# Performance work log

Measured on AMD Instinct MI355X. Metric: run time of the kernel, lower is better.

Reference implementation:

```python
import jax, jax.numpy as jnp
from jax import lax
import numpy as np

N, E = 64, 126            # nodes per graph, directed edges (N = E//2 + 1)
BS, T = 32, 512           # batch, train_seq_len
G = BS * T                # total graphs
IN = N * 2                # encoder input_size
H8 = 128 * 8              # hidden_size * 8
OUT = 128                 # output_size (decoder GRU hidden)
L = 2                     # num_layers


def setup_inputs() -> dict:
    key = jax.random.key(0)
    ks = iter(jax.random.split(key, 64))
    def rn(shape, s=0.05):
        return jax.random.normal(next(ks), shape, dtype=jnp.float32) * s
    inp = {}
    inp['x'] = rn((G, N, 2), 1.0)
    inp['edge_index'] = jax.random.randint(next(ks), (2, E), 0, N)
    # GCN params (GCNConv(2,4), GCNConv(4,2), classifier Linear(2,2))
    inp['gcn_w1'] = rn((2, 4), 0.5); inp['gcn_b1'] = rn((4,))
    inp['gcn_w2'] = rn((4, 2), 0.5); inp['gcn_b2'] = rn((2,))
    inp['gcn_cw'] = rn((2, 2), 0.5); inp['gcn_cb'] = rn((2,))
    # Encoder: fl Linear(IN, H8); GRU(H8, H8, L)
    inp['enc_fl_w'] = rn((IN, H8)); inp['enc_fl_b'] = rn((H8,))
    inp['enc_wih'] = rn((L, 3 * H8, H8)); inp['enc_whh'] = rn((L, 3 * H8, H8))
    inp['enc_bih'] = rn((L, 3 * H8)); inp['enc_bhh'] = rn((L, 3 * H8))
    # Decoder: fl Linear(H8, H8); GRU(H8, OUT, L); Linear(OUT, OUT)
    inp['dec_fl_w'] = rn((H8, H8)); inp['dec_fl_b'] = rn((H8,))
    inp['dec_wih0'] = rn((3 * OUT, H8)); inp['dec_wih1'] = rn((3 * OUT, OUT))
    inp['dec_whh'] = rn((L, 3 * OUT, OUT))
    inp['dec_bih'] = rn((L, 3 * OUT)); inp['dec_bhh'] = rn((L, 3 * OUT))
    inp['dec_lin_w'] = rn((OUT, OUT)); inp['dec_lin_b'] = rn((OUT,))
    return inp


def _gcn_conv(h, src, dst, W, b):
    # PyG GCNConv: self-loops + symmetric normalization. h: [G, N, Fin]
    hw = h @ W                                   # [G, N, Fout]
    deg = jnp.ones((N,), hw.dtype).at[dst].add(jnp.ones((E,), hw.dtype))
    dinv = lax.rsqrt(deg)
    norm = dinv[src] * dinv[dst]                 # [E]
    msgs = hw[:, src, :] * norm[None, :, None]   # gather + scale
    agg = jnp.zeros_like(hw).at[:, dst, :].add(msgs)
    agg = agg + hw * (dinv * dinv)[None, :, None]  # self-loop term (norm = 1/deg)
    return agg + b


def _gru_layer(x_seq, wih, whh, bih, bhh):
    # x_seq: [B, T, D]; torch nn.GRU math, h0 = 0
    B = x_seq.shape[0]
    H = whh.shape[1]
    h0 = jnp.zeros((B, H), x_seq.dtype)
    def step(h, x_t):
        gi = x_t @ wih.T + bih
        gh = h @ whh.T + bhh
        i_r, i_z, i_n = jnp.split(gi, 3, axis=-1)
        h_r, h_z, h_n = jnp.split(gh, 3, axis=-1)
        r = jax.nn.sigmoid(i_r + h_r)
        z = jax.nn.sigmoid(i_z + h_z)
        n = jnp.tanh(i_n + r * h_n)
        h_new = (1.0 - z) * n + z * h
        return h_new, h_new
    _, ys = lax.scan(step, h0, jnp.swapaxes(x_seq, 0, 1))
    return jnp.swapaxes(ys, 0, 1)


def reference(x, edge_index, gcn_w1, gcn_b1, gcn_w2, gcn_b2, gcn_cw, gcn_cb,
              enc_fl_w, enc_fl_b, enc_wih, enc_whh, enc_bih, enc_bhh,
              dec_fl_w, dec_fl_b, dec_wih0, dec_wih1, dec_whh, dec_bih, dec_bhh,
              dec_lin_w, dec_lin_b):
    src, dst = edge_index[0], edge_index[1]
    # GCN over all G graphs at once (vectorizes the per-graph Python loop)
    h = jnp.tanh(_gcn_conv(x, src, dst, gcn_w1, gcn_b1))
    h = jnp.tanh(_gcn_conv(h, src, dst, gcn_w2, gcn_b2))
    h = h @ gcn_cw + gcn_cb                      # [G, N, 2]
    res = h.reshape(BS, T, IN)
    # Encoder
    out = jax.nn.relu(res @ enc_fl_w + enc_fl_b)
    for l in range(L):
        out = _gru_layer(out, enc_wih[l], enc_whh[l], enc_bih[l], enc_bhh[l])
    # Decoder (dropout in eval mode = identity)
    d = jax.nn.relu(out @ dec_fl_w + dec_fl_b)
    d = _gru_layer(d, dec_wih0, dec_whh[0], dec_bih[0], dec_bhh[0])
    d = _gru_layer(d, dec_wih1, dec_whh[1], dec_bih[1], dec_bhh[1])
    return d @ dec_lin_w + dec_lin_b             # [BS, T, OUT]
```

## Files before the change

kernel.cpp:

```cpp
#include <hip/hip_runtime.h>

typedef unsigned short u16;
typedef unsigned long long u64;
typedef __attribute__((ext_vector_type(8))) short bf16x8;
typedef __attribute__((ext_vector_type(4))) float f32x4;

#define BSZ 32
#define TT 512
#define GG (BSZ*TT)
#define NNODE 64
#define EE 126
#define H8 1024
#define H3 3072

__device__ __forceinline__ float b2f(u16 u){
  union { unsigned i; float f; } v; v.i = ((unsigned)u) << 16; return v.f;
}
__device__ __forceinline__ u16 f2b(float f){
  unsigned i = __float_as_uint(f);
  unsigned r = (i + 0x7FFFu + ((i >> 16) & 1u)) >> 16;
  return (u16)r;
}
__device__ __forceinline__ float sigm(float x){ return 1.f/(1.f+__expf(-x)); }
__device__ __forceinline__ float tanh_f(float x){
  float xc = fminf(fmaxf(x, -15.f), 15.f);
  float e = __expf(2.f*xc);
  return (e-1.f)/(e+1.f);
}
__device__ __forceinline__ int prow(int m, int perm){
  return perm ? ((m & (TT-1))*BSZ + (m >> 9)) : m;
}
__device__ __forceinline__ u64 aload64(const u64* p){
  return __hip_atomic_load(p, __ATOMIC_RELAXED, __HIP_MEMORY_SCOPE_AGENT);
}
__device__ __forceinline__ void spin128(int* base, int t){
  for (;;){
    int s = 0;
    #pragma unroll
    for (int i = 0; i < 8; i++)
      s += __hip_atomic_load(&base[i*TT + t], __ATOMIC_RELAXED, __HIP_MEMORY_SCOPE_AGENT);
    if (s == 128) break;
    __builtin_amdgcn_s_sleep(1);
  }
  asm volatile("" ::: "memory");
}

__global__ __launch_bounds__(256) void detect_dtype(const void* xraw, int* flag){
  __shared__ int cnt;
  if (threadIdx.x == 0) cnt = 0;
  __syncthreads();
  const u16* p = (const u16*)xraw;
  u16 u = p[2*threadIdx.x];
  int e = (u >> 7) & 0xFF;
  int weird = (e < 100 || e > 134) ? 1 : 0;
  atomicAdd(&cnt, weird);
  __syncthreads();
  if (threadIdx.x == 0) *flag = (cnt > 128) ? 1 : 0;
}

__global__ __launch_bounds__(256) void cvt_bf16(const void* __restrict__ in,
                                                u16* __restrict__ out, int n,
                                                const int* __restrict__ flag){
  int i = blockIdx.x*256 + threadIdx.x;
  if (i >= n) return;
  if (*flag) out[i] = f2b(((const float*)in)[i]);
  else       out[i] = ((const u16*)in)[i];
}

__global__ __launch_bounds__(64) void gcn_kernel(
    const u16* __restrict__ x, const int* __restrict__ ei,
    const u16* __restrict__ w1, const u16* __restrict__ b1,
    const u16* __restrict__ w2, const u16* __restrict__ b2,
    const u16* __restrict__ cw, const u16* __restrict__ cb,
    u16* __restrict__ res)
{
  __shared__ int se[EE], de[EE];
  __shared__ float dinv[NNODE];
  __shared__ float nrm[EE];
  __shared__ float hs[NNODE][4];
  const int n = threadIdx.x;
  const int g = blockIdx.x;
  for (int e = n; e < EE; e += 64){ se[e] = ei[e]; de[e] = ei[EE + e]; }
  __syncthreads();
  int cnt = 0;
  for (int e = 0; e < EE; e++) cnt += (de[e] == n) ? 1 : 0;
  float di = rsqrtf(1.0f + (float)cnt);
  dinv[n] = di;
  float x0 = b2f(x[((size_t)g*NNODE + n)*2 + 0]);
  float x1 = b2f(x[((size_t)g*NNODE + n)*2 + 1]);
  float hw[4];
  #pragma unroll
  for (int c = 0; c < 4; c++) hw[c] = x0*b2f(w1[c]) + x1*b2f(w1[4+c]);
  #pragma unroll
  for (int c = 0; c < 4; c++) hs[n][c] = hw[c];
  __syncthreads();
  for (int e = n; e < EE; e += 64) nrm[e] = dinv[se[e]] * dinv[de[e]];
  __syncthreads();
  float selfc = di*di;
  float agg[4];
  #pragma unroll
  for (int c = 0; c < 4; c++) agg[c] = hw[c]*selfc;
  for (int e = 0; e < EE; e++){
    if (de[e] == n){
      float w = nrm[e]; int s = se[e];
      #pragma unroll
      for (int c = 0; c < 4; c++) agg[c] += hs[s][c]*w;
    }
  }
  float h1[4];
  #pragma unroll
  for (int c = 0; c < 4; c++) h1[c] = tanh_f(agg[c] + b2f(b1[c]));
  __syncthreads();
  float hw2[2];
  #pragma unroll
  for (int c = 0; c < 2; c++){
    float s = 0.f;
    #pragma unroll
    for (int k = 0; k < 4; k++) s += h1[k]*b2f(w2[k*2+c]);
    hw2[c] = s;
    hs[n][c] = s;
  }
  __syncthreads();
  float agg2[2] = { hw2[0]*selfc, hw2[1]*selfc };
  for (int e = 0; e < EE; e++){
    if (de[e] == n){
      float w = nrm[e]; int s = se[e];
      agg2[0] += hs[s][0]*w;
      agg2[1] += hs[s][1]*w;
    }
  }
  float h2a = tanh_f(agg2[0] + b2f(b2[0]));
  float h2b = tanh_f(agg2[1] + b2f(b2[1]));
  #pragma unroll
  for (int c = 0; c < 2; c++){
    float o = h2a*b2f(cw[c]) + h2b*b2f(cw[2+c]) + b2f(cb[c]);
    res[(size_t)g*128 + n*2 + c] = f2b(o);
  }
}

__global__ __launch_bounds__(256) void transpose_bf16(
    const u16* __restrict__ in, u16* __restrict__ out, int R, int C)
{
  __shared__ u16 tile[32][33];
  int c0 = blockIdx.x*32, r0 = blockIdx.y*32;
  for (int i = threadIdx.y; i < 32; i += 8)
    tile[i][threadIdx.x] = in[(size_t)(r0+i)*C + c0 + threadIdx.x];
  __syncthreads();
  for (int i = threadIdx.y; i < 32; i += 8)
    out[(size_t)(c0+i)*R + r0 + threadIdx.x] = tile[threadIdx.x][i];
}

__global__ __launch_bounds__(256) void gemm_nt(
    const u16* __restrict__ A, const u16* __restrict__ Bm,
    const u16* __restrict__ bias, void* __restrict__ C,
    int M, int N, int K, int relu, int permA, int permC,
    const int* __restrict__ outflag)
{
  const int wave = threadIdx.x >> 6;
  const int lane = threadIdx.x & 63;
  const int wm = wave >> 1, wn = wave & 1;
  const int q = lane >> 4, lr = lane & 15;
  const int mBase = blockIdx.y*128 + wm*64;
  const int nBase = blockIdx.x*128 + wn*64;
  f32x4 acc[4][4] = {};
  const u16* ap[4]; const u16* bp[4];
  #pragma unroll
  for (int i = 0; i < 4; i++){
    ap[i] = A + (size_t)prow(mBase + i*16 + lr, permA)*K + q*8;
    bp[i] = Bm + (size_t)(nBase + i*16 + lr)*K + q*8;
  }
  for (int kb = 0; kb < K; kb += 32){
    bf16x8 av[4], bv[4];
    #pragma unroll
    for (int i = 0; i < 4; i++){
      av[i] = *(const bf16x8*)ap[i]; bv[i] = *(const bf16x8*)bp[i];
      ap[i] += 32; bp[i] += 32;
    }
    #pragma unroll
    for (int mi = 0; mi < 4; mi++)
      #pragma unroll
      for (int ni = 0; ni < 4; ni++)
        acc[mi][ni] = __builtin_amdgcn_mfma_f32_16x16x32_bf16(av[mi], bv[ni], acc[mi][ni], 0, 0, 0);
  }
  const int of32 = outflag ? *outflag : 0;
  #pragma unroll
  for (int ni = 0; ni < 4; ni++){
    int col = nBase + ni*16 + lr;
    float bb = bias ? b2f(bias[col]) : 0.f;
    #pragma unroll
    for (int mi = 0; mi < 4; mi++){
      #pragma unroll
      for (int r = 0; r < 4; r++){
        int row = prow(mBase + mi*16 + q*4 + r, permC);
        float v = acc[mi][ni][r] + bb;
        if (relu) v = fmaxf(v, 0.f);
        size_t idx = (size_t)row*N + col;
        if (of32) ((float*)C)[idx] = v;
        else      ((u16*)C)[idx]   = f2b(v);
      }
    }
  }
}

__global__ __launch_bounds__(64) void enc_pipe(
    const u16* __restrict__ gi,
    const u16* __restrict__ wih1,
    const u16* __restrict__ whh0,
    const u16* __restrict__ whh1,
    const u16* __restrict__ bih1, const u16* __restrict__ bhh0,
    const u16* __restrict__ bhh1,
    u16* __restrict__ h0seq,
    u16* __restrict__ h1seq,
    int* __restrict__ cnt)
{
  const int wid = blockIdx.x;
  const int lane = threadIdx.x & 63;
  const int q = lane >> 4, lr = lane & 15;
  const int sub = wid & 7;
  float hreg[4] = {0.f,0.f,0.f,0.f};
  int* c0 = cnt;
  int* c1 = cnt + 8*TT;

  if (wid < 128){
    const int jg = wid & 63, half = wid >> 6;
    const int j = jg*16 + lr, bbase = half*16;
    const float bh_r = b2f(bhh0[j]);
    const float bh_z = b2f(bhh0[H8 + j]);
    const float bh_n = b2f(bhh0[2*H8 + j]);
    const u16* wp0 = whh0 + (size_t)(0*H8 + j)*H8 + q*8;
    const u16* wp1 = whh0 + (size_t)(1*H8 + j)*H8 + q*8;
    const u16* wp2 = whh0 + (size_t)(2*H8 + j)*H8 + q*8;
    u16 gpre[12];
    #pragma unroll
    for (int r = 0; r < 4; r++){
      size_t row = (size_t)(bbase + q*4 + r)*H3;
      gpre[r]   = gi[row + j];
      gpre[4+r] = gi[row + H8 + j];
      gpre[8+r] = gi[row + 2*H8 + j];
    }
    for (int t = 0; t < TT; t++){
      if (t > 0) spin128(c0, t - 1);
      float gr_[4], gz_[4], gn_[4];
      #pragma unroll
      for (int r = 0; r < 4; r++){
        gr_[r] = b2f(gpre[r]); gz_[r] = b2f(gpre[4+r]); gn_[r] = b2f(gpre[8+r]);
      }
      f32x4 acc0 = {}, acc1 = {}, acc2 = {};
      if (t > 0){
        const u16* ap = h0seq + (size_t)((t-1)*BSZ + bbase + lr)*H8 + q*8;
        #pragma unroll 8
        for (int kb = 0; kb < 32; kb++){
          const u64* p = (const u64*)(ap + kb*32);
          union { u64 v[2]; bf16x8 b; } A; A.v[0] = aload64(p); A.v[1] = aload64(p+1);
          bf16x8 w0 = *(const bf16x8*)(wp0 + kb*32);
          bf16x8 w1 = *(const bf16x8*)(wp1 + kb*32);
          bf16x8 w2 = *(const bf16x8*)(wp2 + kb*32);
          acc0 = __builtin_amdgcn_mfma_f32_16x16x32_bf16(A.b, w0, acc0, 0,0,0);
          acc1 = __builtin_amdgcn_mfma_f32_16x16x32_bf16(A.b, w1, acc1, 0,0,0);
          acc2 = __builtin_amdgcn_mfma_f32_16x16x32_bf16(A.b, w2, acc2, 0,0,0);
        }
      }
      #pragma unroll
      for (int r = 0; r < 4; r++){
        float rr = sigm(gr_[r] + acc0[r] + bh_r);
        float zz = sigm(gz_[r] + acc1[r] + bh_z);
        float nn = tanh_f(gn_[r] + rr*(acc2[r] + bh_n));
        float hnew = (1.f - zz)*nn + zz*hreg[r];
        hreg[r] = hnew;
        __hip_atomic_store(&h0seq[(size_t)(t*BSZ + bbase + q*4 + r)*H8 + j], f2b(hnew),
                           __ATOMIC_RELAXED, __HIP_MEMORY_SCOPE_AGENT);
      }
      asm volatile("s_waitcnt vmcnt(0)" ::: "memory");
      if (lane == 0)
        __hip_atomic_fetch_add(&c0[sub*TT + t], 1, __ATOMIC_RELAXED, __HIP_MEMORY_SCOPE_AGENT);
      if (t + 1 < TT){
        #pragma unroll
        for (int r = 0; r < 4; r++){
          size_t row = (size_t)((t+1)*BSZ + bbase + q*4 + r)*H3;
          gpre[r]   = gi[row + j];
          gpre[4+r] = gi[row + H8 + j];
          gpre[8+r] = gi[row + 2*H8 + j];
        }
      }
    }
  } else {
    const int wid2 = wid - 128;
    const int jg = wid2 & 63, half = wid2 >> 6;
    const int j = jg*16 + lr, bbase = half*16;
    const float bir = b2f(bih1[j]);
    const float biz = b2f(bih1[H8 + j]);
    const float bin = b2f(bih1[2*H8 + j]);
    const float bhr = b2f(bhh1[j]);
    const float bhz = b2f(bhh1[H8 + j]);
    const float bhn = b2f(bhh1[2*H8 + j]);
    const u16* ip0 = wih1 + (size_t)(0*H8 + j)*H8 + q*8;
    const u16* ip1 = wih1 + (size_t)(1*H8 + j)*H8 + q*8;
    const u16* ip2 = wih1 + (size_t)(2*H8 + j)*H8 + q*8;
    const u16* hp0 = whh1 + (size_t)(0*H8 + j)*H8 + q*8;
    const u16* hp1 = whh1 + (size_t)(1*H8 + j)*H8 + q*8;
    const u16* hp2 = whh1 + (size_t)(2*H8 + j)*H8 + q*8;
    for (int t = 0; t < TT; t++){
      spin128(c0, t);
      if (t > 0) spin128(c1, t - 1);
      f32x4 aI0 = {}, aI1 = {}, aI2 = {}, aH0 = {}, aH1 = {}, aH2 = {};
      const u16* a0p = h0seq + (size_t)(t*BSZ + bbase + lr)*H8 + q*8;
      if (t > 0){
        const u16* a1p = h1seq + (size_t)((t-1)*BSZ + bbase + lr)*H8 + q*8;
        #pragma unroll 4
        for (int kb = 0; kb < 32; kb++){
          const u64* p0 = (const u64*)(a0p + kb*32);
          union { u64 v[2]; bf16x8 b; } A0; A0.v[0] = aload64(p0); A0.v[1] = aload64(p0+1);
          const u64* p1 = (const u64*)(a1p + kb*32);
          union { u64 v[2]; bf16x8 b; } A1; A1.v[0] = aload64(p1); A1.v[1] = aload64(p1+1);
          bf16x8 i0 = *(const bf16x8*)(ip0 + kb*32);
          bf16x8 i1 = *(const bf16x8*)(ip1 + kb*32);
          bf16x8 i2 = *(const bf16x8*)(ip2 + kb*32);
          bf16x8 h0v = *(const bf16x8*)(hp0 + kb*32);
          bf16x8 h1v = *(const bf16x8*)(hp1 + kb*32);
          bf16x8 h2v = *(const bf16x8*)(hp2 + kb*32);
          aI0 = __builtin_amdgcn_mfma_f32_16x16x32_bf16(A0.b, i0, aI0, 0,0,0);
          aI1 = __builtin_amdgcn_mfma_f32_16x16x32_bf16(A0.b, i1, aI1, 0,0,0);
          aI2 = __builtin_amdgcn_mfma_f32_16x16x32_bf16(A0.b, i2, aI2, 0,0,0);
          aH0 = __builtin_amdgcn_mfma_f32_16x16x32_bf16(A1.b, h0v, aH0, 0,0,0);
          aH1 = __builtin_amdgcn_mfma_f32_16x16x32_bf16(A1.b, h1v, aH1, 0,0,0);
          aH2 = __builtin_amdgcn_mfma_f32_16x16x32_bf16(A1.b, h2v, aH2, 0,0,0);
        }
      } else {
        #pragma unroll 8
        for (int kb = 0; kb < 32; kb++){
          const u64* p0 = (const u64*)(a0p + kb*32);
          union { u64 v[2]; bf16x8 b; } A0; A0.v[0] = aload64(p0); A0.v[1] = aload64(p0+1);
          bf16x8 i0 = *(const bf16x8*)(ip0 + kb*32);
          bf16x8 i1 = *(const bf16x8*)(ip1 + kb*32);
          bf16x8 i2 = *(const bf16x8*)(ip2 + kb*32);
          aI0 = __builtin_amdgcn_mfma_f32_16x16x32_bf16(A0.b, i0, aI0, 0,0,0);
          aI1 = __builtin_amdgcn_mfma_f32_16x16x32_bf16(A0.b, i1, aI1, 0,0,0);
          aI2 = __builtin_amdgcn_mfma_f32_16x16x32_bf16(A0.b, i2, aI2, 0,0,0);
        }
      }
      #pragma unroll
      for (int r = 0; r < 4; r++){
        float rr = sigm(aI0[r] + bir + aH0[r] + bhr);
        float zz = sigm(aI1[r] + biz + aH1[r] + bhz);
        float nn = tanh_f(aI2[r] + bin + rr*(aH2[r] + bhn));
        float hnew = (1.f - zz)*nn + zz*hreg[r];
        hreg[r] = hnew;
        __hip_atomic_store(&h1seq[(size_t)(t*BSZ + bbase + q*4 + r)*H8 + j], f2b(hnew),
                           __ATOMIC_RELAXED, __HIP_MEMORY_SCOPE_AGENT);
      }
      asm volatile("s_waitcnt vmcnt(0)" ::: "memory");
      if (lane == 0)
        __hip_atomic_fetch_add(&c1[sub*TT + t], 1, __ATOMIC_RELAXED, __HIP_MEMORY_SCOPE_AGENT);
    }
  }
}

__global__ __launch_bounds__(256) void dec_rec(
    const u16* __restrict__ gi,
    const u16* __restrict__ whh,
    const u16* __restrict__ bhh,
    u16* __restrict__ seq)
{
  __shared__ u16 hlds[16*136];
  const int bb = blockIdx.x*16;
  const int tid = threadIdx.x;
  const int w = tid >> 6, lane = tid & 63, q = lane >> 4, lr = lane & 15;
  bf16x8 wreg[3][2][4];
  #pragma unroll
  for (int g2 = 0; g2 < 3; g2++)
    #pragma unroll
    for (int nt = 0; nt < 2; nt++){
      int jj = g2*128 + w*32 + nt*16 + lr;
      #pragma unroll
      for (int kb = 0; kb < 4; kb++)
        wreg[g2][nt][kb] = *(const bf16x8*)(whh + (size_t)jj*128 + kb*32 + q*8);
    }
  float bh[3][2];
  #pragma unroll
  for (int g2 = 0; g2 < 3; g2++)
    #pragma unroll
    for (int nt = 0; nt < 2; nt++)
      bh[g2][nt] = b2f(bhh[g2*128 + w*32 + nt*16 + lr]);
  float hreg[2][4] = {};
  u16 gpre[3][2][4];
  #pragma unroll
  for (int r = 0; r < 4; r++){
    size_t row = (size_t)(bb + q*4 + r)*384;
    #pragma unroll
    for (int nt = 0; nt < 2; nt++){
      int jj = w*32 + nt*16 + lr;
      #pragma unroll
      for (int g2 = 0; g2 < 3; g2++)
        gpre[g2][nt][r] = gi[row + g2*128 + jj];
    }
  }
  __syncthreads();
  for (int t = 0; t < TT; t++){
    float gif[3][2][4];
    #pragma unroll
    for (int g2 = 0; g2 < 3; g2++)
      #pragma unroll
      for (int nt = 0; nt < 2; nt++)
        #pragma unroll
        for (int r = 0; r < 4; r++)
          gif[g2][nt][r] = b2f(gpre[g2][nt][r]);
    f32x4 acc[3][2] = {};
    if (t > 0){
      #pragma unroll
      for (int kb = 0; kb < 4; kb++){
        bf16x8 a = *(const bf16x8*)(hlds + lr*136 + kb*32 + q*8);
        #pragma unroll
        for (int g2 = 0; g2 < 3; g2++)
          #pragma unroll
          for (int nt = 0; nt < 2; nt++)
            acc[g2][nt] = __builtin_amdgcn_mfma_f32_16x16x32_bf16(a, wreg[g2][nt][kb], acc[g2][nt], 0,0,0);
      }
    }
    __syncthreads();
    #pragma unroll
    for (int nt = 0; nt < 2; nt++)
      #pragma unroll
      for (int r = 0; r < 4; r++){
        int jj = w*32 + nt*16 + lr;
        int b = bb + q*4 + r;
        float rr = sigm(gif[0][nt][r] + acc[0][nt][r] + bh[0][nt]);
        float zz = sigm(gif[1][nt][r] + acc[1][nt][r] + bh[1][nt]);
        float nn = tanh_f(gif[2][nt][r] + rr*(acc[2][nt][r] + bh[2][nt]));
        float hnew = (1.f - zz)*nn + zz*hreg[nt][r];
        hreg[nt][r] = hnew;
        u16 hb = f2b(hnew);
        hlds[(q*4 + r)*136 + jj] = hb;
        seq[(size_t)(t*BSZ + b)*128 + jj] = hb;
      }
    if (t + 1 < TT){
      #pragma unroll
      for (int r = 0; r < 4; r++){
        size_t row = (size_t)((t+1)*BSZ + bb + q*4 + r)*384;
        #pragma unroll
        for (int nt = 0; nt < 2; nt++){
          int jj = w*32 + nt*16 + lr;
          #pragma unroll
          for (int g2 = 0; g2 < 3; g2++)
            gpre[g2][nt][r] = gi[row + g2*128 + jj];
        }
      }
    }
    __syncthreads();
  }
}

extern "C" void kernel_launch(void* const* d_in, const int* in_sizes, int n_in,
                              void* d_out, int out_size, void* d_ws, size_t ws_size,
                              hipStream_t stream)
{
  const void* x    = d_in[0];
  const int* ei    = (const int*)d_in[1];

  const size_t NEED = (size_t)164 << 20;
  if (ws_size < NEED) return;
  char* wsb = (char*)d_ws;
  const size_t KB = 1024, MB = 1024*1024;

  int* syncv = (int*)wsb;
  int* flag  = (int*)(wsb + 40*KB);
  u16* gw1_c  = (u16*)(wsb + 1*MB + 0);
  u16* gb1_c  = (u16*)(wsb + 1*MB + 64);
  u16* gw2_c  = (u16*)(wsb + 1*MB + 128);
  u16* gb2_c  = (u16*)(wsb + 1*MB + 192);
  u16* gcw_c  = (u16*)(wsb + 1*MB + 256);
  u16* gcb_c  = (u16*)(wsb + 1*MB + 320);
  u16* efb_c  = (u16*)(wsb + 1*MB + 4*KB);
  u16* ebih_c = (u16*)(wsb + 1*MB + 8*KB);
  u16* ebhh_c = (u16*)(wsb + 1*MB + 24*KB);
  u16* dfb_c  = (u16*)(wsb + 1*MB + 40*KB);
  u16* dbih_c = (u16*)(wsb + 1*MB + 45*KB);
  u16* dbhh_c = (u16*)(wsb + 1*MB + 47*KB);
  u16* dlb_c  = (u16*)(wsb + 1*MB + 49*KB);
  u16* wT3    = (u16*)(wsb + 1*MB + 64*KB);
  u16* dlw_c  = (u16*)(wsb + 1*MB + 128*KB);
  u16* efw_c  = (u16*)(wsb + 1*MB + 192*KB);
  u16* wT1    = (u16*)(wsb + 1*MB + 448*KB);
  u16* dfw_c  = (u16*)(wsb + 2*MB);
  u16* wT2    = (u16*)(wsb + 4*MB);
  u16* dwih0_c= (u16*)(wsb + 6*MB);
  u16* dwih1_c= (u16*)(wsb + 7*MB);
  u16* dwhh_c = (u16*)(wsb + 7*MB + 128*KB);
  u16* ewih_c = (u16*)(wsb + 8*MB);
  u16* ewhh_c = (u16*)(wsb + 20*MB);
  u16* res    = (u16*)(wsb + 32*MB);
  u16* bufA   = (u16*)(wsb + 36*MB);
  u16* bufC   = (u16*)(wsb + 68*MB);
  u16* x_c    = bufC;
  u16* h1seq  = bufC;
  u16* d0     = (u16*)(wsb + 102*MB);
  u16* giD    = (u16*)(wsb + 136*MB);

  hipMemsetAsync(syncv, 0, 32*KB, stream);
  detect_dtype<<<1, 256, 0, stream>>>(x, flag);

  auto cvt = [&](int idx, u16* dst, int n){
    cvt_bf16<<<(n + 255)/256, 256, 0, stream>>>(d_in[idx], dst, n, flag);
  };
  cvt(0,  x_c,     GG*NNODE*2);
  cvt(2,  gw1_c, 8);  cvt(3, gb1_c, 4);  cvt(4, gw2_c, 8);
  cvt(5,  gb2_c, 2);  cvt(6, gcw_c, 4);  cvt(7, gcb_c, 2);
  cvt(8,  efw_c,   128*1024);   cvt(9,  efb_c, 1024);
  cvt(10, ewih_c,  2*3072*1024);
  cvt(11, ewhh_c,  2*3072*1024);
  cvt(12, ebih_c,  2*3072);     cvt(13, ebhh_c, 2*3072);
  cvt(14, dfw_c,   1024*1024);  cvt(15, dfb_c, 1024);
  cvt(16, dwih0_c, 384*1024);   cvt(17, dwih1_c, 384*128);
  cvt(18, dwhh_c,  2*384*128);
  cvt(19, dbih_c,  2*384);      cvt(20, dbhh_c, 2*384);
  cvt(21, dlw_c,   128*128);    cvt(22, dlb_c, 128);

  transpose_bf16<<<dim3(1024/32, 128/32),  dim3(32,8), 0, stream>>>(efw_c, wT1, 128, 1024);
  transpose_bf16<<<dim3(1024/32, 1024/32), dim3(32,8), 0, stream>>>(dfw_c, wT2, 1024, 1024);
  transpose_bf16<<<dim3(128/32, 128/32),   dim3(32,8), 0, stream>>>(dlw_c, wT3, 128, 128);

  gcn_kernel<<<GG, 64, 0, stream>>>(x_c, ei, gw1_c, gb1_c, gw2_c, gb2_c, gcw_c, gcb_c, res);

  gemm_nt<<<dim3(1024/128, GG/128), 256, 0, stream>>>(res, wT1, efb_c, bufA, GG, 1024, 128, 1, 0, 1, nullptr);
  gemm_nt<<<dim3(3072/128, GG/128), 256, 0, stream>>>(bufA, ewih_c, ebih_c, bufC, GG, 3072, 1024, 0, 1, 1, nullptr);
  enc_pipe<<<256, 64, 0, stream>>>(bufC, ewih_c + 3072*1024, ewhh_c, ewhh_c + 3072*1024,
                                   ebih_c + 3072, ebhh_c, ebhh_c + 3072,
                                   bufA, h1seq, syncv);

  gemm_nt<<<dim3(1024/128, GG/128), 256, 0, stream>>>(h1seq, wT2, dfb_c, d0, GG, 1024, 1024, 1, 1, 1, nullptr);
  gemm_nt<<<dim3(384/128, GG/128), 256, 0, stream>>>(d0, dwih0_c, dbih_c, giD, GG, 384, 1024, 0, 1, 1, nullptr);
  dec_rec<<<2, 256, 0, stream>>>(giD, dwhh_c, dbhh_c, res);
  gemm_nt<<<dim3(384/128, GG/128), 256, 0, stream>>>(res, dwih1_c, dbih_c + 384, giD, GG, 384, 128, 0, 1, 1, nullptr);
  dec_rec<<<2, 256, 0, stream>>>(giD, dwhh_c + 384*128, dbhh_c + 384, bufA);

  gemm_nt<<<dim3(128/128, GG/128), 256, 0, stream>>>(bufA, wT3, dlb_c, d_out, GG, 128, 128, 0, 1, 0, flag);
}
```

Measured before the change: 11.72 ms.

## Compute layer-1 input projection before waiting on previous hidden state

In the fused encoder GRU kernel, layer-1 warps now run the input-side MFMA pass over the layer-0 output before spinning on the layer-1 counter for step t-1. Only the recurrent-side pass waits on that counter. The r and z gates share accumulators across the input and hidden products, and their biases are pre-summed. This takes the input projection off the serial recurrence critical path, at the cost of two separate loops in place of one interleaved loop.

```diff
diff --git a/kernel.cpp b/kernel.cpp
--- a/kernel.cpp
+++ b/kernel.cpp
@@ -287,12 +287,10 @@
     const int wid2 = wid - 128;
     const int jg = wid2 & 63, half = wid2 >> 6;
     const int j = jg*16 + lr, bbase = half*16;
-    const float bir = b2f(bih1[j]);
-    const float biz = b2f(bih1[H8 + j]);
-    const float bin = b2f(bih1[2*H8 + j]);
-    const float bhr = b2f(bhh1[j]);
-    const float bhz = b2f(bhh1[H8 + j]);
-    const float bhn = b2f(bhh1[2*H8 + j]);
+    const float brz_r = b2f(bih1[j])        + b2f(bhh1[j]);
+    const float brz_z = b2f(bih1[H8 + j])   + b2f(bhh1[H8 + j]);
+    const float bin   = b2f(bih1[2*H8 + j]);
+    const float bhn   = b2f(bhh1[2*H8 + j]);
     const u16* ip0 = wih1 + (size_t)(0*H8 + j)*H8 + q*8;
     const u16* ip1 = wih1 + (size_t)(1*H8 + j)*H8 + q*8;
     const u16* ip2 = wih1 + (size_t)(2*H8 + j)*H8 + q*8;
@@ -301,47 +299,38 @@
     const u16* hp2 = whh1 + (size_t)(2*H8 + j)*H8 + q*8;
     for (int t = 0; t < TT; t++){
       spin128(c0, t);
-      if (t > 0) spin128(c1, t - 1);
-      f32x4 aI0 = {}, aI1 = {}, aI2 = {}, aH0 = {}, aH1 = {}, aH2 = {};
+      f32x4 accR = {}, accZ = {}, aI2 = {}, aH2 = {};
       const u16* a0p = h0seq + (size_t)(t*BSZ + bbase + lr)*H8 + q*8;
+      #pragma unroll 8
+      for (int kb = 0; kb < 32; kb++){
+        const u64* p0 = (const u64*)(a0p + kb*32);
+        union { u64 v[2]; bf16x8 b; } A0; A0.v[0] = aload64(p0); A0.v[1] = aload64(p0+1);
+        bf16x8 i0 = *(const bf16x8*)(ip0 + kb*32);
+        bf16x8 i1 = *(const bf16x8*)(ip1 + kb*32);
+        bf16x8 i2 = *(const bf16x8*)(ip2 + kb*32);
+        accR = __builtin_amdgcn_mfma_f32_16x16x32_bf16(A0.b, i0, accR, 0,0,0);
+        accZ = __builtin_amdgcn_mfma_f32_16x16x32_bf16(A0.b, i1, accZ, 0,0,0);
+        aI2  = __builtin_amdgcn_mfma_f32_16x16x32_bf16(A0.b, i2, aI2,  0,0,0);
+      }
       if (t > 0){
+        spin128(c1, t - 1);
         const u16* a1p = h1seq + (size_t)((t-1)*BSZ + bbase + lr)*H8 + q*8;
-        #pragma unroll 4
+        #pragma unroll 8
         for (int kb = 0; kb < 32; kb++){
-          const u64* p0 = (const u64*)(a0p + kb*32);
-          union { u64 v[2]; bf16x8 b; } A0; A0.v[0] = aload64(p0); A0.v[1] = aload64(p0+1);
           const u64* p1 = (const u64*)(a1p + kb*32);
           union { u64 v[2]; bf16x8 b; } A1; A1.v[0] = aload64(p1); A1.v[1] = aload64(p1+1);
-          bf16x8 i0 = *(const bf16x8*)(ip0 + kb*32);
-          bf16x8 i1 = *(const bf16x8*)(ip1 + kb*32);
-          bf16x8 i2 = *(const bf16x8*)(ip2 + kb*32);
           bf16x8 h0v = *(const bf16x8*)(hp0 + kb*32);
           bf16x8 h1v = *(const bf16x8*)(hp1 + kb*32);
           bf16x8 h2v = *(const bf16x8*)(hp2 + kb*32);
-          aI0 = __builtin_amdgcn_mfma_f32_16x16x32_bf16(A0.b, i0, aI0, 0,0,0);
-          aI1 = __builtin_amdgcn_mfma_f32_16x16x32_bf16(A0.b, i1, aI1, 0,0,0);
-          aI2 = __builtin_amdgcn_mfma_f32_16x16x32_bf16(A0.b, i2, aI2, 0,0,0);
-          aH0 = __builtin_amdgcn_mfma_f32_16x16x32_bf16(A1.b, h0v, aH0, 0,0,0);
-          aH1 = __builtin_amdgcn_mfma_f32_16x16x32_bf16(A1.b, h1v, aH1, 0,0,0);
-          aH2 = __builtin_amdgcn_mfma_f32_16x16x32_bf16(A1.b, h2v, aH2, 0,0,0);
+          accR = __builtin_amdgcn_mfma_f32_16x16x32_bf16(A1.b, h0v, accR, 0,0,0);
+          accZ = __builtin_amdgcn_mfma_f32_16x16x32_bf16(A1.b, h1v, accZ, 0,0,0);
+          aH2  = __builtin_amdgcn_mfma_f32_16x16x32_bf16(A1.b, h2v, aH2,  0,0,0);
         }
-      } else {
-        #pragma unroll 8
-        for (int kb = 0; kb < 32; kb++){
-          const u64* p0 = (const u64*)(a0p + kb*32);
-          union { u64 v[2]; bf16x8 b; } A0; A0.v[0] = aload64(p0); A0.v[1] = aload64(p0+1);
-          bf16x8 i0 = *(const bf16x8*)(ip0 + kb*32);
-          bf16x8 i1 = *(const bf16x8*)(ip1 + kb*32);
-          bf16x8 i2 = *(const bf16x8*)(ip2 + kb*32);
-          aI0 = __builtin_amdgcn_mfma_f32_16x16x32_bf16(A0.b, i0, aI0, 0,0,0);
-          aI1 = __builtin_amdgcn_mfma_f32_16x16x32_bf16(A0.b, i1, aI1, 0,0,0);
-          aI2 = __builtin_amdgcn_mfma_f32_16x16x32_bf16(A0.b, i2, aI2, 0,0,0);
-        }
       }
       #pragma unroll
       for (int r = 0; r < 4; r++){
-        float rr = sigm(aI0[r] + bir + aH0[r] + bhr);
-        float zz = sigm(aI1[r] + biz + aH1[r] + bhz);
+        float rr = sigm(accR[r] + brz_r);
+        float zz = sigm(accZ[r] + brz_z);
         float nn = tanh_f(aI2[r] + bin + rr*(aH2[r] + bhn));
         float hnew = (1.f - zz)*nn + zz*hreg[r];
         hreg[r] = hnew;
```

New measurement: 10.83 ms. -7.6%, faster.
